# Optimization experiments

Measured on AMD Instinct MI355X. Metric: run time of the kernel, lower is better.

## Reference

```python
import jax, jax.numpy as jnp
import numpy as np

C_IN, C_OUT, K = 64, 64, 3
KK = K * K


def _conv3x3(x, w, b):
    # x: [B, Cin, H, W], w: [Cout, Cin, 3, 3], b: [Cout] or None. stride 1, pad 1.
    y = jax.lax.conv_general_dilated(
        x, w, window_strides=(1, 1), padding=((1, 1), (1, 1)),
        dimension_numbers=("NCHW", "OIHW", "NCHW"))
    if b is not None:
        y = y + b[None, :, None, None]
    return y


def _deform_conv2d(x, offset, mask, weight):
    # torchvision.ops.deform_conv2d with stride=1, pad=1, dilation=1, 1 offset group.
    # x: [B,C,H,W]; offset: [B,2*KK,H,W] (per-tap (dy,dx)); mask: [B,KK,H,W];
    # weight: [O,C,K,K]
    B, C, H, W = x.shape
    O = weight.shape[0]
    ky, kx = jnp.meshgrid(jnp.arange(K), jnp.arange(K), indexing="ij")
    hs = jnp.arange(H)
    ws = jnp.arange(W)
    # base sample positions per tap k=(ky*K+kx): [KK,H,W]
    base_y = (hs[:, None] - 1)[None] + ky.reshape(KK, 1, 1)
    base_x = (ws[None, :] - 1)[None] + kx.reshape(KK, 1, 1)
    off = offset.reshape(B, KK, 2, H, W)
    py = base_y[None].astype(x.dtype) + off[:, :, 0]  # [B,KK,H,W]
    px = base_x[None].astype(x.dtype) + off[:, :, 1]

    y0 = jnp.floor(py)
    x0 = jnp.floor(px)
    wy = py - y0  # bilinear fractional weights
    wx = px - x0
    y0i = y0.astype(jnp.int32)
    x0i = x0.astype(jnp.int32)

    imflat = x.reshape(B, C, H * W)

    def gather_b(im, idx):  # im: [C,HW], idx: [KK,H,W] -> [C,KK,H,W]
        return im[:, idx]

    val = jnp.zeros((B, C, KK, H, W), x.dtype)
    for dy, dx in ((0, 0), (0, 1), (1, 0), (1, 1)):
        yc = y0i + dy
        xc = x0i + dx
        valid = ((yc >= 0) & (yc < H) & (xc >= 0) & (xc < W)).astype(x.dtype)
        cw = (wy if dy else (1.0 - wy)) * (wx if dx else (1.0 - wx)) * valid
        idx = jnp.clip(yc, 0, H - 1) * W + jnp.clip(xc, 0, W - 1)
        g = jax.vmap(gather_b)(imflat, idx)  # [B,C,KK,H,W]
        val = val + cw[:, None] * g
    val = val * mask[:, None]  # modulation
    # contract 9-tap patches with conv weight
    return jnp.einsum("bckhw,ock->bohw", val, weight.reshape(O, C, KK))


def setup_inputs() -> dict:
    key = jax.random.key(0)
    ks = jax.random.split(key, 8)
    B, H, W = 4, 96, 96
    cin2 = 2 * C_IN + 2
    frame_i = jax.random.normal(ks[0], (B, C_IN, H, W), jnp.float32)
    frame_j = jax.random.normal(ks[1], (B, C_IN, H, W), jnp.float32)
    flow_ij = jax.random.normal(ks[2], (B, 2, H, W), jnp.float32)
    # small random weights so offsets are nonzero (zero-init would degenerate)
    w_off = jax.random.normal(ks[3], (2 * KK, cin2, K, K), jnp.float32) * 0.01
    b_off = jax.random.normal(ks[4], (2 * KK,), jnp.float32) * 0.1
    w_mod = jax.random.normal(ks[5], (KK, cin2, K, K), jnp.float32) * 0.01
    b_mod = jax.random.normal(ks[6], (KK,), jnp.float32) * 0.1
    w_reg = jax.random.normal(ks[7], (C_OUT, C_IN, K, K), jnp.float32) * (1.0 / np.sqrt(C_IN * KK))
    return {"frame_i": frame_i, "frame_j": frame_j, "flow_ij": flow_ij,
            "w_off": w_off, "b_off": b_off, "w_mod": w_mod, "b_mod": b_mod,
            "w_reg": w_reg}


def reference(frame_i, frame_j, flow_ij, w_off, b_off, w_mod, b_mod, w_reg):
    offset_input = jnp.concatenate([frame_i, frame_j, flow_ij], axis=1)
    offset = _conv3x3(offset_input, w_off, b_off)            # [B,2*KK,H,W]
    modulator = 2.0 * jax.nn.sigmoid(_conv3x3(offset_input, w_mod, b_mod))  # [B,KK,H,W]
    return _deform_conv2d(frame_j, offset, modulator, w_reg)
```

## Files before the change

kernel.cpp:

```cpp
#include <hip/hip_runtime.h>
#include <math.h>

#define BB   4
#define HH   96
#define WW   96
#define HW   (HH * WW)
#define CIN  64
#define COUT 64
#define C2B  192
#define NROW (BB * HW)
#define ZROW NROW
#define NSTRIP (NROW / 16)
#define BPX3 (NSTRIP / 8)
#define NA   (9 * 5 * 2 * 512)
#define NW   (9 * 2 * 4 * 512)
#define PXB2 (NROW / 32)
#define PWBLK 324
#define TSX  35
#define PR   55

typedef short v8s __attribute__((ext_vector_type(8)));
typedef float v4f __attribute__((ext_vector_type(4)));

__device__ __forceinline__ unsigned short f2bf(float f) {
    unsigned u = __float_as_uint(f);
    return (unsigned short)((u + 0x7FFFu + ((u >> 16) & 1u)) >> 16);
}
__device__ __forceinline__ unsigned pack2(float a, float b) {
    return (unsigned)f2bf(a) | ((unsigned)f2bf(b) << 16);
}
__device__ __forceinline__ unsigned bil2(unsigned a, unsigned b, unsigned c,
                                         unsigned d, float w00, float w01,
                                         float w10, float w11) {
    float lo = w00 * __uint_as_float(a << 16) + w01 * __uint_as_float(b << 16)
             + w10 * __uint_as_float(c << 16) + w11 * __uint_as_float(d << 16);
    float hi = w00 * __uint_as_float(a & 0xffff0000u)
             + w01 * __uint_as_float(b & 0xffff0000u)
             + w10 * __uint_as_float(c & 0xffff0000u)
             + w11 * __uint_as_float(d & 0xffff0000u);
    return pack2(lo, hi);
}

__global__ __launch_bounds__(256) void prep_kernel(
    const float* __restrict__ fi, const float* __restrict__ fj,
    const float* __restrict__ fl, const float* __restrict__ w_off,
    const float* __restrict__ w_mod, const float* __restrict__ w_reg,
    unsigned short* __restrict__ xt, unsigned short* __restrict__ wa2f,
    unsigned short* __restrict__ wb2f, uint4* __restrict__ vt)
{
    int blk = blockIdx.x;
    if (blk < PXB2) {
        __shared__ __align__(16) unsigned tile[64 * TSX];
        int tid = threadIdx.x;
        int p = tid & 63, cg = tid >> 6;
        int u = blk >> 1, half = blk & 1;
        int r0 = u * 64;
        int b = r0 / HW;
        int hwb = r0 - b * HW;
        int hw = hwb + p;
        uint4* dst = (uint4*)(xt + (size_t)r0 * C2B);
        if (half == 0) {
            const float* pi = fi + (size_t)b * CIN * HW + hw;
#pragma unroll
            for (int d = 0; d < 8; ++d) {
                int c = cg * 16 + 2 * d;
                tile[p * TSX + cg * 8 + d] =
                    pack2(pi[(size_t)c * HW], pi[(size_t)(c + 1) * HW]);
            }
            __syncthreads();
#pragma unroll
            for (int i = 0; i < 2; ++i) {
                int gq = i * 256 + tid;
                int rl = gq >> 3, c4 = gq & 7;
                const unsigned* s = &tile[rl * TSX + c4 * 4];
                uint4 v = {s[0], s[1], s[2], s[3]};
                dst[rl * 24 + c4] = v;
            }
        } else {
            const float* pj = fj + (size_t)b * CIN * HW + hw;
#pragma unroll
            for (int d = 0; d < 8; ++d) {
                int c = cg * 16 + 2 * d;
                tile[p * TSX + cg * 8 + d] =
                    pack2(pj[(size_t)c * HW], pj[(size_t)(c + 1) * HW]);
            }
            if (cg == 0) {
                const float* pf = fl + (size_t)b * 2 * HW + hw;
                tile[p * TSX + 32] = pack2(pf[0], pf[HW]);
            }
            __syncthreads();
#pragma unroll
            for (int i = 0; i < 4; ++i) {
                int gq = i * 256 + tid;
                int rl = gq >> 4, c4 = gq & 15;
                uint4 v = {0u, 0u, 0u, 0u};
                if (c4 < 8) {
                    const unsigned* s = &tile[rl * TSX + c4 * 4];
                    v.x = s[0]; v.y = s[1]; v.z = s[2]; v.w = s[3];
                } else if (c4 == 8) {
                    v.x = tile[rl * TSX + 32];
                }
                int pc4 = (c4 < 8) ? ((c4 & 3) * 2 + (c4 >> 2)) : c4;
                dst[rl * 24 + 8 + pc4] = v;
            }
#pragma unroll
            for (int i = 0; i < 2; ++i) {
                int it = i * 256 + tid;
                int pl = it >> 6, rl = it & 63;
                int o  = (pl >> 1) + (pl & 1) * 4;
                const unsigned* s = &tile[rl * TSX + o * 4];
                uint4 v = {s[0], s[1], s[2], s[3]};
                vt[((size_t)(b * 8 + pl)) * HW + hwb + rl] = v;
            }
        }
    } else if (blk < PXB2 + PWBLK) {
        int e = (blk - PXB2) * 256 + threadIdx.x;
        if (e < NA) {
            int t  = e / 5120;
            int r1 = e - t * 5120;
            int ks = r1 >> 10;
            int r2 = r1 & 1023;
            int nt = r2 >> 9;
            int l9 = r2 & 511;
            int l  = l9 >> 3, ee = l9 & 7;
            int m  = l & 15, g = l >> 4;
            int oc = nt * 16 + m;
            int ch = ks * 32 + g * 8 + ee;
            float v = 0.0f;
            if (oc < 27 && ch < 130) {
                if (oc < 18) v = w_off[((size_t)oc * 130 + ch) * 9 + t];
                else         v = w_mod[((size_t)(oc - 18) * 130 + ch) * 9 + t];
            }
            wa2f[e] = f2bf(v);
        } else {
            int e2 = e - NA;
            if (e2 < NW) {
                int k  = e2 >> 12;
                int r1 = e2 & 4095;
                int ks = r1 >> 11;
                int r2 = r1 & 2047;
                int nt = r2 >> 9;
                int l9 = r2 & 511;
                int l  = l9 >> 3, ee = l9 & 7;
                int m  = l & 15, g = l >> 4;
                int o  = nt * 16 + m;
                int c  = ks * 32 + g * 8 + ee;
                wb2f[e2] = f2bf(w_reg[((size_t)o * 64 + c) * 9 + k]);
            }
        }
    } else {
        if (threadIdx.x < 24) {
            uint4 z = {0u, 0u, 0u, 0u};
            ((uint4*)(xt + (size_t)ZROW * C2B))[threadIdx.x] = z;
        }
    }
}

__global__ __launch_bounds__(512, 8) void fused_kernel(
    const unsigned short* __restrict__ xt,
    const unsigned short* __restrict__ wa2f,
    const unsigned short* __restrict__ wb2f,
    const uint4* __restrict__ vt,
    const float* __restrict__ b_off, const float* __restrict__ b_mod,
    float* __restrict__ out)
{
    __shared__ __align__(16) unsigned char pool[17600];
    __shared__ __align__(16) float red1[8][8][64];
    __shared__ float lraw[16 * 28];

    uint4* patch4 = (uint4*)pool;
    float* red2   = (float*)pool;

    int l = threadIdx.x & 63;
    int wid = __builtin_amdgcn_readfirstlane(threadIdx.x >> 6);
    int m = l & 15, g = l >> 4;
    int strip = (blockIdx.x & 7) * BPX3 + (blockIdx.x >> 3);
    int b = strip / (HW / 16);
    int hw0 = (strip - b * (HW / 16)) * 16;
    int hw = hw0 + m;
    int x = hw % WW, y = hw / WW;
    int y0b = hw0 / WW, x0b = hw0 - y0b * WW;

#pragma unroll
    for (int i = 0; i < 3; ++i) {
        int item = i * 512 + threadIdx.x;
        if (item < 1080) {
            int run = item / 360;
            int rem = item - run * 360;
            int r18 = rem / 20;
            int c8  = rem - r18 * 20;
            int yy = y0b + run - 1;
            int xx = x0b - 1 + r18;
            bool ok = ((unsigned)yy < HH) && ((unsigned)xx < WW);
            uint4 v = {0u, 0u, 0u, 0u};
            if (ok)
                v = ((const uint4*)(xt + (size_t)(b * HW + yy * WW + xx) * C2B))[c8];
            patch4[c8 * PR + run * 18 + r18] = v;
        }
    }
    __syncthreads();

    v4f acc0 = {0.f, 0.f, 0.f, 0.f};
    v4f acc1 = {0.f, 0.f, 0.f, 0.f};
    {
        int nu = (wid < 5) ? 6 : 5;
#pragma unroll
        for (int i = 0; i < 6; ++i) {
            if (i < nu) {
                int u = wid + 8 * i;
                int t = u / 5, ks = u - 5 * t;
                int r = (t / 3) * 18 + (t % 3) + m;
                int c8 = (ks == 0) ? g : (ks == 1) ? 4 + g
                       : (ks == 2) ? 8 + 2 * g : (ks == 3) ? 9 + 2 * g
                       : 16 + g;
                v8s a = *(const v8s*)&patch4[c8 * PR + r];
                const unsigned short* wp =
                    wa2f + ((size_t)(u * 2)) * 512 + l * 8;
                v8s b0 = *(const v8s*)(wp);
                v8s b1 = *(const v8s*)(wp + 512);
                acc0 = __builtin_amdgcn_mfma_f32_16x16x32_bf16(a, b0, acc0, 0, 0, 0);
                acc1 = __builtin_amdgcn_mfma_f32_16x16x32_bf16(a, b1, acc1, 0, 0, 0);
            }
        }
    }

    {
#pragma unroll
        for (int j = 0; j < 4; ++j) red1[wid][j][l] = acc0[j];
#pragma unroll
        for (int j = 0; j < 4; ++j) red1[wid][4 + j][l] = acc1[j];
    }
    __syncthreads();

    {
        int j = wid;
        float v = 0.f;
#pragma unroll
        for (int sw = 0; sw < 8; ++sw) v += red1[sw][j][l];
        int r = j & 3;
        int oc = (j < 4) ? m : 16 + m;
        int pos = g * 4 + r;
        if (oc < 18) {
            lraw[pos * 28 + oc] = v + b_off[oc];
        } else if (oc < 27) {
            lraw[pos * 28 + oc] =
                2.0f / (1.0f + __expf(-(v + b_mod[oc - 18])));
        }
    }
    __syncthreads();

    v4f acc[4];
#pragma unroll
    for (int nt = 0; nt < 4; ++nt) acc[nt] = (v4f){0.f, 0.f, 0.f, 0.f};

    auto do_tap = [&](int k) {
        int ky = k / 3, kx = k - 3 * ky;
        float dy = lraw[m * 28 + 2 * k];
        float dx = lraw[m * 28 + 2 * k + 1];
        float mm = lraw[m * 28 + 18 + k];

        float py = (float)(y - 1 + ky) + dy;
        float px = (float)(x - 1 + kx) + dx;
        float fy = floorf(py), fx = floorf(px);
        int   y0 = (int)fy,    x0 = (int)fx;
        float wy = py - fy,    wx = px - fx;
        int   y1 = y0 + 1,     x1 = x0 + 1;

        bool y0v = (y0 >= 0) && (y0 < HH);
        bool y1v = (y1 >= 0) && (y1 < HH);
        bool x0v = (x0 >= 0) && (x0 < WW);
        bool x1v = (x1 >= 0) && (x1 < WW);

        float w00 = (1.f - wy) * (1.f - wx) * ((y0v && x0v) ? mm : 0.f);
        float w01 = (1.f - wy) * wx         * ((y0v && x1v) ? mm : 0.f);
        float w10 = wy * (1.f - wx)         * ((y1v && x0v) ? mm : 0.f);
        float w11 = wy * wx                 * ((y1v && x1v) ? mm : 0.f);

        int y0c = min(max(y0, 0), HH - 1), y1c = min(max(y1, 0), HH - 1);
        int x0c = min(max(x0, 0), WW - 1), x1c = min(max(x1, 0), WW - 1);
        int i00 = y0c * WW + x0c, i01 = y0c * WW + x1c;
        int i10 = y1c * WW + x0c, i11 = y1c * WW + x1c;

        const uint4* p0 = vt + ((size_t)(b * 8 + 2 * g + 0)) * HW;
        const uint4* p1 = vt + ((size_t)(b * 8 + 2 * g + 1)) * HW;

        uint4 a00 = p0[i00];
        uint4 a01 = p0[i01];
        uint4 a10 = p0[i10];
        uint4 a11 = p0[i11];
        uint4 c00 = p1[i00];
        uint4 c01 = p1[i01];
        uint4 c10 = p1[i10];
        uint4 c11 = p1[i11];

        uint4 ov0, ov1;
        ov0.x = bil2(a00.x, a01.x, a10.x, a11.x, w00, w01, w10, w11);
        ov0.y = bil2(a00.y, a01.y, a10.y, a11.y, w00, w01, w10, w11);
        ov0.z = bil2(a00.z, a01.z, a10.z, a11.z, w00, w01, w10, w11);
        ov0.w = bil2(a00.w, a01.w, a10.w, a11.w, w00, w01, w10, w11);
        ov1.x = bil2(c00.x, c01.x, c10.x, c11.x, w00, w01, w10, w11);
        ov1.y = bil2(c00.y, c01.y, c10.y, c11.y, w00, w01, w10, w11);
        ov1.z = bil2(c00.z, c01.z, c10.z, c11.z, w00, w01, w10, w11);
        ov1.w = bil2(c00.w, c01.w, c10.w, c11.w, w00, w01, w10, w11);
        v8s af0 = __builtin_bit_cast(v8s, ov0);
        v8s af1 = __builtin_bit_cast(v8s, ov1);

#pragma unroll
        for (int nt = 0; nt < 4; ++nt) {
            const unsigned short* wp0 =
                wb2f + ((size_t)((k * 2 + 0) * 4 + nt)) * 512 + l * 8;
            const unsigned short* wp1 =
                wb2f + ((size_t)((k * 2 + 1) * 4 + nt)) * 512 + l * 8;
            v8s bb0 = *(const v8s*)wp0;
            v8s bb1 = *(const v8s*)wp1;
            acc[nt] = __builtin_amdgcn_mfma_f32_16x16x32_bf16(af0, bb0, acc[nt], 0, 0, 0);
            acc[nt] = __builtin_amdgcn_mfma_f32_16x16x32_bf16(af1, bb1, acc[nt], 0, 0, 0);
        }
    };

    auto do_half = [&](int k, int ks) {
        int ky = k / 3, kx = k - 3 * ky;
        float dy = lraw[m * 28 + 2 * k];
        float dx = lraw[m * 28 + 2 * k + 1];
        float mm = lraw[m * 28 + 18 + k];

        float py = (float)(y - 1 + ky) + dy;
        float px = (float)(x - 1 + kx) + dx;
        float fy = floorf(py), fx = floorf(px);
        int   y0 = (int)fy,    x0 = (int)fx;
        float wy = py - fy,    wx = px - fx;
        int   y1 = y0 + 1,     x1 = x0 + 1;

        bool y0v = (y0 >= 0) && (y0 < HH);
        bool y1v = (y1 >= 0) && (y1 < HH);
        bool x0v = (x0 >= 0) && (x0 < WW);
        bool x1v = (x1 >= 0) && (x1 < WW);

        float w00 = (1.f - wy) * (1.f - wx) * ((y0v && x0v) ? mm : 0.f);
        float w01 = (1.f - wy) * wx         * ((y0v && x1v) ? mm : 0.f);
        float w10 = wy * (1.f - wx)         * ((y1v && x0v) ? mm : 0.f);
        float w11 = wy * wx                 * ((y1v && x1v) ? mm : 0.f);

        int y0c = min(max(y0, 0), HH - 1), y1c = min(max(y1, 0), HH - 1);
        int x0c = min(max(x0, 0), WW - 1), x1c = min(max(x1, 0), WW - 1);
        int i00 = y0c * WW + x0c, i01 = y0c * WW + x1c;
        int i10 = y1c * WW + x0c, i11 = y1c * WW + x1c;

        const uint4* pk = vt + ((size_t)(b * 8 + 2 * g + ks)) * HW;
        uint4 a00 = pk[i00];
        uint4 a01 = pk[i01];
        uint4 a10 = pk[i10];
        uint4 a11 = pk[i11];

        uint4 ov;
        ov.x = bil2(a00.x, a01.x, a10.x, a11.x, w00, w01, w10, w11);
        ov.y = bil2(a00.y, a01.y, a10.y, a11.y, w00, w01, w10, w11);
        ov.z = bil2(a00.z, a01.z, a10.z, a11.z, w00, w01, w10, w11);
        ov.w = bil2(a00.w, a01.w, a10.w, a11.w, w00, w01, w10, w11);
        v8s af = __builtin_bit_cast(v8s, ov);

#pragma unroll
        for (int nt = 0; nt < 4; ++nt) {
            const unsigned short* wp =
                wb2f + ((size_t)((k * 2 + ks) * 4 + nt)) * 512 + l * 8;
            v8s bb = *(const v8s*)wp;
            acc[nt] = __builtin_amdgcn_mfma_f32_16x16x32_bf16(af, bb, acc[nt], 0, 0, 0);
        }
    };

    do_tap(wid);
    if (wid == 6) do_half(8, 0);
    if (wid == 7) do_half(8, 1);

    if (wid >= 4) {
        float* rb = red2 + ((size_t)(wid - 4) * 16) * 64;
#pragma unroll
        for (int nt = 0; nt < 4; ++nt)
#pragma unroll
            for (int r = 0; r < 4; ++r)
                rb[(nt * 4 + r) * 64 + l] = acc[nt][r];
    }
    __syncthreads();
    if (wid < 4) {
        float* rb = red2 + ((size_t)wid * 16) * 64;
#pragma unroll
        for (int nt = 0; nt < 4; ++nt)
#pragma unroll
            for (int r = 0; r < 4; ++r) {
                float t = rb[(nt * 4 + r) * 64 + l] + acc[nt][r];
                rb[(nt * 4 + r) * 64 + l] = t;
            }
    }
    __syncthreads();
    {
        int nt = wid >> 1, r0 = (wid & 1) * 2;
        float v0 = 0.f, v1 = 0.f;
#pragma unroll
        for (int bu = 0; bu < 4; ++bu) {
            v0 += red2[((size_t)bu * 16 + nt * 4 + r0) * 64 + l];
            v1 += red2[((size_t)bu * 16 + nt * 4 + r0 + 1) * 64 + l];
        }
        float* op = out + ((size_t)(b * COUT + nt * 16 + m)) * HW
                  + hw0 + g * 4 + r0;
        float2 s2 = {v0, v1};
        *(float2*)op = s2;
    }
}

extern "C" void kernel_launch(void* const* d_in, const int* in_sizes, int n_in,
                              void* d_out, int out_size, void* d_ws, size_t ws_size,
                              hipStream_t stream)
{
    const float* frame_i = (const float*)d_in[0];
    const float* frame_j = (const float*)d_in[1];
    const float* flow_ij = (const float*)d_in[2];
    const float* w_off   = (const float*)d_in[3];
    const float* b_off   = (const float*)d_in[4];
    const float* w_mod   = (const float*)d_in[5];
    const float* b_mod   = (const float*)d_in[6];
    const float* w_reg   = (const float*)d_in[7];
    float* out = (float*)d_out;

    unsigned short* xt   = (unsigned short*)d_ws;
    unsigned short* wa2f = xt + (size_t)(NROW + 1) * C2B;
    unsigned short* wb2f = wa2f + NA;
    uint4* vt            = (uint4*)(wb2f + NW);

    prep_kernel<<<PXB2 + PWBLK + 1, 256, 0, stream>>>(
        frame_i, frame_j, flow_ij, w_off, w_mod, w_reg, xt, wa2f, wb2f, vt);

    fused_kernel<<<NSTRIP, 512, 0, stream>>>(
        xt, wa2f, wb2f, vt, b_off, b_mod, out);
}
```

Baseline: 115.3 us.

## Make fused kernel persistent over three strips with register-prefetched patches

The fused kernel now launches 768 blocks, each handling three 16-pixel strips in a loop instead of one strip per block. The input patch for the next strip is loaded into registers while the current strip computes, so global load latency overlaps with MFMA and gather work. The cost is extra registers for the prefetch (launch bounds lowered from 8 to 6), an extra barrier per iteration, and less parallelism across blocks.

Result: slower. 202.9 us (+76.0%).

```diff
diff --git a/kernel.cpp b/kernel.cpp
--- a/kernel.cpp
+++ b/kernel.cpp
@@ -12,6 +12,7 @@
 #define ZROW NROW
 #define NSTRIP (NROW / 16)
 #define BPX3 (NSTRIP / 8)
+#define GRID 768
 #define NA   (9 * 5 * 2 * 512)
 #define NW   (9 * 2 * 4 * 512)
 #define PXB2 (NROW / 32)
@@ -156,7 +157,7 @@
     }
 }
 
-__global__ __launch_bounds__(512, 8) void fused_kernel(
+__global__ __launch_bounds__(512, 6) void fused_kernel(
     const unsigned short* __restrict__ xt,
     const unsigned short* __restrict__ wa2f,
     const unsigned short* __restrict__ wb2f,
@@ -171,239 +172,275 @@
     uint4* patch4 = (uint4*)pool;
     float* red2   = (float*)pool;
 
-    int l = threadIdx.x & 63;
-    int wid = __builtin_amdgcn_readfirstlane(threadIdx.x >> 6);
+    int tid = threadIdx.x;
+    int l = tid & 63;
+    int wid = __builtin_amdgcn_readfirstlane(tid >> 6);
     int m = l & 15, g = l >> 4;
-    int strip = (blockIdx.x & 7) * BPX3 + (blockIdx.x >> 3);
-    int b = strip / (HW / 16);
-    int hw0 = (strip - b * (HW / 16)) * 16;
-    int hw = hw0 + m;
-    int x = hw % WW, y = hw / WW;
-    int y0b = hw0 / WW, x0b = hw0 - y0b * WW;
-
-#pragma unroll
+    int bx = blockIdx.x;
+
+    int it0 = tid, it1 = tid + 512, it2 = tid + 1024;
+    int run0 = it0 / 360, rm0 = it0 - run0 * 360;
+    int r180 = rm0 / 20,  c80 = rm0 - r180 * 20;
+    int run1 = it1 / 360, rm1 = it1 - run1 * 360;
+    int r181 = rm1 / 20,  c81 = rm1 - r181 * 20;
+    int run2 = it2 / 360, rm2 = it2 - run2 * 360;
+    int r182 = rm2 / 20,  c82 = rm2 - r182 * 20;
+    int lo0 = c80 * PR + run0 * 18 + r180;
+    int lo1 = c81 * PR + run1 * 18 + r181;
+    int lo2 = c82 * PR + run2 * 18 + r182;
+
+    auto ld_item = [&](int b, int y0b, int x0b, int run, int r18, int c8) {
+        int yy = y0b + run - 1;
+        int xx = x0b - 1 + r18;
+        bool ok = ((unsigned)yy < HH) && ((unsigned)xx < WW);
+        uint4 v = {0u, 0u, 0u, 0u};
+        if (ok)
+            v = ((const uint4*)(xt + (size_t)(b * HW + yy * WW + xx) * C2B))[c8];
+        return v;
+    };
+
+    auto geom = [&](int sj, int& b, int& hw0) {
+        int strip = (sj & 7) * BPX3 + (sj >> 3);
+        b = strip / (HW / 16);
+        hw0 = (strip - b * (HW / 16)) * 16;
+    };
+
+    uint4 pf0, pf1, pf2;
+    {
+        int b, hw0; geom(bx, b, hw0);
+        int y0b = hw0 / WW, x0b = hw0 - y0b * WW;
+        pf0 = ld_item(b, y0b, x0b, run0, r180, c80);
+        pf1 = ld_item(b, y0b, x0b, run1, r181, c81);
+        pf2 = (tid < 56) ? ld_item(b, y0b, x0b, run2, r182, c82)
+                         : (uint4){0u, 0u, 0u, 0u};
+    }
+
+#pragma unroll 1
     for (int i = 0; i < 3; ++i) {
-        int item = i * 512 + threadIdx.x;
-        if (item < 1080) {
-            int run = item / 360;
-            int rem = item - run * 360;
-            int r18 = rem / 20;
-            int c8  = rem - r18 * 20;
-            int yy = y0b + run - 1;
-            int xx = x0b - 1 + r18;
-            bool ok = ((unsigned)yy < HH) && ((unsigned)xx < WW);
-            uint4 v = {0u, 0u, 0u, 0u};
-            if (ok)
-                v = ((const uint4*)(xt + (size_t)(b * HW + yy * WW + xx) * C2B))[c8];
-            patch4[c8 * PR + run * 18 + r18] = v;
-        }
-    }
-    __syncthreads();
-
-    v4f acc0 = {0.f, 0.f, 0.f, 0.f};
-    v4f acc1 = {0.f, 0.f, 0.f, 0.f};
-    {
-        int nu = (wid < 5) ? 6 : 5;
-#pragma unroll
-        for (int i = 0; i < 6; ++i) {
-            if (i < nu) {
-                int u = wid + 8 * i;
-                int t = u / 5, ks = u - 5 * t;
-                int r = (t / 3) * 18 + (t % 3) + m;
-                int c8 = (ks == 0) ? g : (ks == 1) ? 4 + g
-                       : (ks == 2) ? 8 + 2 * g : (ks == 3) ? 9 + 2 * g
-                       : 16 + g;
-                v8s a = *(const v8s*)&patch4[c8 * PR + r];
+        int sj = bx + i * GRID;
+        int b, hw0; geom(sj, b, hw0);
+        int hw = hw0 + m;
+        int x = hw % WW, y = hw / WW;
+
+        patch4[lo0] = pf0;
+        patch4[lo1] = pf1;
+        if (tid < 56) patch4[lo2] = pf2;
+        __syncthreads();
+
+        if (i < 2) {
+            int bn, hn; geom(sj + GRID, bn, hn);
+            int y0n = hn / WW, x0n = hn - y0n * WW;
+            pf0 = ld_item(bn, y0n, x0n, run0, r180, c80);
+            pf1 = ld_item(bn, y0n, x0n, run1, r181, c81);
+            if (tid < 56) pf2 = ld_item(bn, y0n, x0n, run2, r182, c82);
+        }
+
+        v4f acc0 = {0.f, 0.f, 0.f, 0.f};
+        v4f acc1 = {0.f, 0.f, 0.f, 0.f};
+        {
+            int nu = (wid < 5) ? 6 : 5;
+#pragma unroll
+            for (int ii = 0; ii < 6; ++ii) {
+                if (ii < nu) {
+                    int u = wid + 8 * ii;
+                    int t = u / 5, ks = u - 5 * t;
+                    int r = (t / 3) * 18 + (t % 3) + m;
+                    int c8 = (ks == 0) ? g : (ks == 1) ? 4 + g
+                           : (ks == 2) ? 8 + 2 * g : (ks == 3) ? 9 + 2 * g
+                           : 16 + g;
+                    v8s a = *(const v8s*)&patch4[c8 * PR + r];
+                    const unsigned short* wp =
+                        wa2f + ((size_t)(u * 2)) * 512 + l * 8;
+                    v8s b0 = *(const v8s*)(wp);
+                    v8s b1 = *(const v8s*)(wp + 512);
+                    acc0 = __builtin_amdgcn_mfma_f32_16x16x32_bf16(a, b0, acc0, 0, 0, 0);
+                    acc1 = __builtin_amdgcn_mfma_f32_16x16x32_bf16(a, b1, acc1, 0, 0, 0);
+                }
+            }
+        }
+
+        {
+#pragma unroll
+            for (int j = 0; j < 4; ++j) red1[wid][j][l] = acc0[j];
+#pragma unroll
+            for (int j = 0; j < 4; ++j) red1[wid][4 + j][l] = acc1[j];
+        }
+        __syncthreads();
+
+        {
+            int j = wid;
+            float v = 0.f;
+#pragma unroll
+            for (int sw = 0; sw < 8; ++sw) v += red1[sw][j][l];
+            int r = j & 3;
+            int oc = (j < 4) ? m : 16 + m;
+            int pos = g * 4 + r;
+            if (oc < 18) {
+                lraw[pos * 28 + oc] = v + b_off[oc];
+            } else if (oc < 27) {
+                lraw[pos * 28 + oc] =
+                    2.0f / (1.0f + __expf(-(v + b_mod[oc - 18])));
+            }
+        }
+        __syncthreads();
+
+        v4f acc[4];
+#pragma unroll
+        for (int nt = 0; nt < 4; ++nt) acc[nt] = (v4f){0.f, 0.f, 0.f, 0.f};
+
+        auto do_tap = [&](int k) {
+            int ky = k / 3, kx = k - 3 * ky;
+            float dy = lraw[m * 28 + 2 * k];
+            float dx = lraw[m * 28 + 2 * k + 1];
+            float mm = lraw[m * 28 + 18 + k];
+
+            float py = (float)(y - 1 + ky) + dy;
+            float px = (float)(x - 1 + kx) + dx;
+            float fy = floorf(py), fx = floorf(px);
+            int   y0 = (int)fy,    x0 = (int)fx;
+            float wy = py - fy,    wx = px - fx;
+            int   y1 = y0 + 1,     x1 = x0 + 1;
+
+            bool y0v = (y0 >= 0) && (y0 < HH);
+            bool y1v = (y1 >= 0) && (y1 < HH);
+            bool x0v = (x0 >= 0) && (x0 < WW);
+            bool x1v = (x1 >= 0) && (x1 < WW);
+
+            float w00 = (1.f - wy) * (1.f - wx) * ((y0v && x0v) ? mm : 0.f);
+            float w01 = (1.f - wy) * wx         * ((y0v && x1v) ? mm : 0.f);
+            float w10 = wy * (1.f - wx)         * ((y1v && x0v) ? mm : 0.f);
+            float w11 = wy * wx                 * ((y1v && x1v) ? mm : 0.f);
+
+            int y0c = min(max(y0, 0), HH - 1), y1c = min(max(y1, 0), HH - 1);
+            int x0c = min(max(x0, 0), WW - 1), x1c = min(max(x1, 0), WW - 1);
+            int i00 = y0c * WW + x0c, i01 = y0c * WW + x1c;
+            int i10 = y1c * WW + x0c, i11 = y1c * WW + x1c;
+
+            const uint4* p0 = vt + ((size_t)(b * 8 + 2 * g + 0)) * HW;
+            const uint4* p1 = vt + ((size_t)(b * 8 + 2 * g + 1)) * HW;
+
+            uint4 a00 = p0[i00];
+            uint4 a01 = p0[i01];
+            uint4 a10 = p0[i10];
+            uint4 a11 = p0[i11];
+            uint4 c00 = p1[i00];
+            uint4 c01 = p1[i01];
+            uint4 c10 = p1[i10];
+            uint4 c11 = p1[i11];
+
+            uint4 ov0, ov1;
+            ov0.x = bil2(a00.x, a01.x, a10.x, a11.x, w00, w01, w10, w11);
+            ov0.y = bil2(a00.y, a01.y, a10.y, a11.y, w00, w01, w10, w11);
+            ov0.z = bil2(a00.z, a01.z, a10.z, a11.z, w00, w01, w10, w11);
+            ov0.w = bil2(a00.w, a01.w, a10.w, a11.w, w00, w01, w10, w11);
+            ov1.x = bil2(c00.x, c01.x, c10.x, c11.x, w00, w01, w10, w11);
+            ov1.y = bil2(c00.y, c01.y, c10.y, c11.y, w00, w01, w10, w11);
+            ov1.z = bil2(c00.z, c01.z, c10.z, c11.z, w00, w01, w10, w11);
+            ov1.w = bil2(c00.w, c01.w, c10.w, c11.w, w00, w01, w10, w11);
+            v8s af0 = __builtin_bit_cast(v8s, ov0);
+            v8s af1 = __builtin_bit_cast(v8s, ov1);
+
+#pragma unroll
+            for (int nt = 0; nt < 4; ++nt) {
+                const unsigned short* wp0 =
+                    wb2f + ((size_t)((k * 2 + 0) * 4 + nt)) * 512 + l * 8;
+                const unsigned short* wp1 =
+                    wb2f + ((size_t)((k * 2 + 1) * 4 + nt)) * 512 + l * 8;
+                v8s bb0 = *(const v8s*)wp0;
+                v8s bb1 = *(const v8s*)wp1;
+                acc[nt] = __builtin_amdgcn_mfma_f32_16x16x32_bf16(af0, bb0, acc[nt], 0, 0, 0);
+                acc[nt] = __builtin_amdgcn_mfma_f32_16x16x32_bf16(af1, bb1, acc[nt], 0, 0, 0);
+            }
+        };
+
+        auto do_half = [&](int k, int ks) {
+            int ky = k / 3, kx = k - 3 * ky;
+            float dy = lraw[m * 28 + 2 * k];
+            float dx = lraw[m * 28 + 2 * k + 1];
+            float mm = lraw[m * 28 + 18 + k];
+
+            float py = (float)(y - 1 + ky) + dy;
+            float px = (float)(x - 1 + kx) + dx;
+            float fy = floorf(py), fx = floorf(px);
+            int   y0 = (int)fy,    x0 = (int)fx;
+            float wy = py - fy,    wx = px - fx;
+            int   y1 = y0 + 1,     x1 = x0 + 1;
+
+            bool y0v = (y0 >= 0) && (y0 < HH);
+            bool y1v = (y1 >= 0) && (y1 < HH);
+            bool x0v = (x0 >= 0) && (x0 < WW);
+            bool x1v = (x1 >= 0) && (x1 < WW);
+
+            float w00 = (1.f - wy) * (1.f - wx) * ((y0v && x0v) ? mm : 0.f);
+            float w01 = (1.f - wy) * wx         * ((y0v && x1v) ? mm : 0.f);
+            float w10 = wy * (1.f - wx)         * ((y1v && x0v) ? mm : 0.f);
+            float w11 = wy * wx                 * ((y1v && x1v) ? mm : 0.f);
+
+            int y0c = min(max(y0, 0), HH - 1), y1c = min(max(y1, 0), HH - 1);
+            int x0c = min(max(x0, 0), WW - 1), x1c = min(max(x1, 0), WW - 1);
+            int i00 = y0c * WW + x0c, i01 = y0c * WW + x1c;
+            int i10 = y1c * WW + x0c, i11 = y1c * WW + x1c;
+
+            const uint4* pk = vt + ((size_t)(b * 8 + 2 * g + ks)) * HW;
+            uint4 a00 = pk[i00];
+            uint4 a01 = pk[i01];
+            uint4 a10 = pk[i10];
+            uint4 a11 = pk[i11];
+
+            uint4 ov;
+            ov.x = bil2(a00.x, a01.x, a10.x, a11.x, w00, w01, w10, w11);
+            ov.y = bil2(a00.y, a01.y, a10.y, a11.y, w00, w01, w10, w11);
+            ov.z = bil2(a00.z, a01.z, a10.z, a11.z, w00, w01, w10, w11);
+            ov.w = bil2(a00.w, a01.w, a10.w, a11.w, w00, w01, w10, w11);
+            v8s af = __builtin_bit_cast(v8s, ov);
+
+#pragma unroll
+            for (int nt = 0; nt < 4; ++nt) {
                 const unsigned short* wp =
-                    wa2f + ((size_t)(u * 2)) * 512 + l * 8;
-                v8s b0 = *(const v8s*)(wp);
-                v8s b1 = *(const v8s*)(wp + 512);
-                acc0 = __builtin_amdgcn_mfma_f32_16x16x32_bf16(a, b0, acc0, 0, 0, 0);
-                acc1 = __builtin_amdgcn_mfma_f32_16x16x32_bf16(a, b1, acc1, 0, 0, 0);
-            }
-        }
-    }
-
-    {
-#pragma unroll
-        for (int j = 0; j < 4; ++j) red1[wid][j][l] = acc0[j];
-#pragma unroll
-        for (int j = 0; j < 4; ++j) red1[wid][4 + j][l] = acc1[j];
-    }
-    __syncthreads();
-
-    {
-        int j = wid;
-        float v = 0.f;
-#pragma unroll
-        for (int sw = 0; sw < 8; ++sw) v += red1[sw][j][l];
-        int r = j & 3;
-        int oc = (j < 4) ? m : 16 + m;
-        int pos = g * 4 + r;
-        if (oc < 18) {
-            lraw[pos * 28 + oc] = v + b_off[oc];
-        } else if (oc < 27) {
-            lraw[pos * 28 + oc] =
-                2.0f / (1.0f + __expf(-(v + b_mod[oc - 18])));
-        }
-    }
-    __syncthreads();
-
-    v4f acc[4];
-#pragma unroll
-    for (int nt = 0; nt < 4; ++nt) acc[nt] = (v4f){0.f, 0.f, 0.f, 0.f};
-
-    auto do_tap = [&](int k) {
-        int ky = k / 3, kx = k - 3 * ky;
-        float dy = lraw[m * 28 + 2 * k];
-        float dx = lraw[m * 28 + 2 * k + 1];
-        float mm = lraw[m * 28 + 18 + k];
-
-        float py = (float)(y - 1 + ky) + dy;
-        float px = (float)(x - 1 + kx) + dx;
-        float fy = floorf(py), fx = floorf(px);
-        int   y0 = (int)fy,    x0 = (int)fx;
-        float wy = py - fy,    wx = px - fx;
-        int   y1 = y0 + 1,     x1 = x0 + 1;
-
-        bool y0v = (y0 >= 0) && (y0 < HH);
-        bool y1v = (y1 >= 0) && (y1 < HH);
-        bool x0v = (x0 >= 0) && (x0 < WW);
-        bool x1v = (x1 >= 0) && (x1 < WW);
-
-        float w00 = (1.f - wy) * (1.f - wx) * ((y0v && x0v) ? mm : 0.f);
-        float w01 = (1.f - wy) * wx         * ((y0v && x1v) ? mm : 0.f);
-        float w10 = wy * (1.f - wx)         * ((y1v && x0v) ? mm : 0.f);
-        float w11 = wy * wx                 * ((y1v && x1v) ? mm : 0.f);
-
-        int y0c = min(max(y0, 0), HH - 1), y1c = min(max(y1, 0), HH - 1);
-        int x0c = min(max(x0, 0), WW - 1), x1c = min(max(x1, 0), WW - 1);
-        int i00 = y0c * WW + x0c, i01 = y0c * WW + x1c;
-        int i10 = y1c * WW + x0c, i11 = y1c * WW + x1c;
-
-        const uint4* p0 = vt + ((size_t)(b * 8 + 2 * g + 0)) * HW;
-        const uint4* p1 = vt + ((size_t)(b * 8 + 2 * g + 1)) * HW;
-
-        uint4 a00 = p0[i00];
-        uint4 a01 = p0[i01];
-        uint4 a10 = p0[i10];
-        uint4 a11 = p0[i11];
-        uint4 c00 = p1[i00];
-        uint4 c01 = p1[i01];
-        uint4 c10 = p1[i10];
-        uint4 c11 = p1[i11];
-
-        uint4 ov0, ov1;
-        ov0.x = bil2(a00.x, a01.x, a10.x, a11.x, w00, w01, w10, w11);
-        ov0.y = bil2(a00.y, a01.y, a10.y, a11.y, w00, w01, w10, w11);
-        ov0.z = bil2(a00.z, a01.z, a10.z, a11.z, w00, w01, w10, w11);
-        ov0.w = bil2(a00.w, a01.w, a10.w, a11.w, w00, w01, w10, w11);
-        ov1.x = bil2(c00.x, c01.x, c10.x, c11.x, w00, w01, w10, w11);
-        ov1.y = bil2(c00.y, c01.y, c10.y, c11.y, w00, w01, w10, w11);
-        ov1.z = bil2(c00.z, c01.z, c10.z, c11.z, w00, w01, w10, w11);
-        ov1.w = bil2(c00.w, c01.w, c10.w, c11.w, w00, w01, w10, w11);
-        v8s af0 = __builtin_bit_cast(v8s, ov0);
-        v8s af1 = __builtin_bit_cast(v8s, ov1);
-
-#pragma unroll
-        for (int nt = 0; nt < 4; ++nt) {
-            const unsigned short* wp0 =
-                wb2f + ((size_t)((k * 2 + 0) * 4 + nt)) * 512 + l * 8;
-            const unsigned short* wp1 =
-                wb2f + ((size_t)((k * 2 + 1) * 4 + nt)) * 512 + l * 8;
-            v8s bb0 = *(const v8s*)wp0;
-            v8s bb1 = *(const v8s*)wp1;
-            acc[nt] = __builtin_amdgcn_mfma_f32_16x16x32_bf16(af0, bb0, acc[nt], 0, 0, 0);
-            acc[nt] = __builtin_amdgcn_mfma_f32_16x16x32_bf16(af1, bb1, acc[nt], 0, 0, 0);
-        }
-    };
-
-    auto do_half = [&](int k, int ks) {
-        int ky = k / 3, kx = k - 3 * ky;
-        float dy = lraw[m * 28 + 2 * k];
-        float dx = lraw[m * 28 + 2 * k + 1];
-        float mm = lraw[m * 28 + 18 + k];
-
-        float py = (float)(y - 1 + ky) + dy;
-        float px = (float)(x - 1 + kx) + dx;
-        float fy = floorf(py), fx = floorf(px);
-        int   y0 = (int)fy,    x0 = (int)fx;
-        float wy = py - fy,    wx = px - fx;
-        int   y1 = y0 + 1,     x1 = x0 + 1;
-
-        bool y0v = (y0 >= 0) && (y0 < HH);
-        bool y1v = (y1 >= 0) && (y1 < HH);
-        bool x0v = (x0 >= 0) && (x0 < WW);
-        bool x1v = (x1 >= 0) && (x1 < WW);
-
-        float w00 = (1.f - wy) * (1.f - wx) * ((y0v && x0v) ? mm : 0.f);
-        float w01 = (1.f - wy) * wx         * ((y0v && x1v) ? mm : 0.f);
-        float w10 = wy * (1.f - wx)         * ((y1v && x0v) ? mm : 0.f);
-        float w11 = wy * wx                 * ((y1v && x1v) ? mm : 0.f);
-
-        int y0c = min(max(y0, 0), HH - 1), y1c = min(max(y1, 0), HH - 1);
-        int x0c = min(max(x0, 0), WW - 1), x1c = min(max(x1, 0), WW - 1);
-        int i00 = y0c * WW + x0c, i01 = y0c * WW + x1c;
-        int i10 = y1c * WW + x0c, i11 = y1c * WW + x1c;
-
-        const uint4* pk = vt + ((size_t)(b * 8 + 2 * g + ks)) * HW;
-        uint4 a00 = pk[i00];
-        uint4 a01 = pk[i01];
-        uint4 a10 = pk[i10];
-        uint4 a11 = pk[i11];
-
-        uint4 ov;
-        ov.x = bil2(a00.x, a01.x, a10.x, a11.x, w00, w01, w10, w11);
-        ov.y = bil2(a00.y, a01.y, a10.y, a11.y, w00, w01, w10, w11);
-        ov.z = bil2(a00.z, a01.z, a10.z, a11.z, w00, w01, w10, w11);
-        ov.w = bil2(a00.w, a01.w, a10.w, a11.w, w00, w01, w10, w11);
-        v8s af = __builtin_bit_cast(v8s, ov);
-
-#pragma unroll
-        for (int nt = 0; nt < 4; ++nt) {
-            const unsigned short* wp =
-                wb2f + ((size_t)((k * 2 + ks) * 4 + nt)) * 512 + l * 8;
-            v8s bb = *(const v8s*)wp;
-            acc[nt] = __builtin_amdgcn_mfma_f32_16x16x32_bf16(af, bb, acc[nt], 0, 0, 0);
-        }
-    };
-
-    do_tap(wid);
-    if (wid == 6) do_half(8, 0);
-    if (wid == 7) do_half(8, 1);
-
-    if (wid >= 4) {
-        float* rb = red2 + ((size_t)(wid - 4) * 16) * 64;
-#pragma unroll
-        for (int nt = 0; nt < 4; ++nt)
-#pragma unroll
-            for (int r = 0; r < 4; ++r)
-                rb[(nt * 4 + r) * 64 + l] = acc[nt][r];
-    }
-    __syncthreads();
-    if (wid < 4) {
-        float* rb = red2 + ((size_t)wid * 16) * 64;
-#pragma unroll
-        for (int nt = 0; nt < 4; ++nt)
-#pragma unroll
-            for (int r = 0; r < 4; ++r) {
-                float t = rb[(nt * 4 + r) * 64 + l] + acc[nt][r];
-                rb[(nt * 4 + r) * 64 + l] = t;
-            }
-    }
-    __syncthreads();
-    {
-        int nt = wid >> 1, r0 = (wid & 1) * 2;
-        float v0 = 0.f, v1 = 0.f;
-#pragma unroll
-        for (int bu = 0; bu < 4; ++bu) {
-            v0 += red2[((size_t)bu * 16 + nt * 4 + r0) * 64 + l];
-            v1 += red2[((size_t)bu * 16 + nt * 4 + r0 + 1) * 64 + l];
-        }
-        float* op = out + ((size_t)(b * COUT + nt * 16 + m)) * HW
-                  + hw0 + g * 4 + r0;
-        float2 s2 = {v0, v1};
-        *(float2*)op = s2;
+                    wb2f + ((size_t)((k * 2 + ks) * 4 + nt)) * 512 + l * 8;
+                v8s bb = *(const v8s*)wp;
+                acc[nt] = __builtin_amdgcn_mfma_f32_16x16x32_bf16(af, bb, acc[nt], 0, 0, 0);
+            }
+        };
+
+        do_tap(wid);
+        if (wid == 6) do_half(8, 0);
+        if (wid == 7) do_half(8, 1);
+
+        if (wid >= 4) {
+            float* rb = red2 + ((size_t)(wid - 4) * 16) * 64;
+#pragma unroll
+            for (int nt = 0; nt < 4; ++nt)
+#pragma unroll
+                for (int r = 0; r < 4; ++r)
+                    rb[(nt * 4 + r) * 64 + l] = acc[nt][r];
+        }
+        __syncthreads();
+        if (wid < 4) {
+            float* rb = red2 + ((size_t)wid * 16) * 64;
+#pragma unroll
+            for (int nt = 0; nt < 4; ++nt)
+#pragma unroll
+                for (int r = 0; r < 4; ++r) {
+                    float t = rb[(nt * 4 + r) * 64 + l] + acc[nt][r];
+                    rb[(nt * 4 + r) * 64 + l] = t;
+                }
+        }
+        __syncthreads();
+        {
+            int nt = wid >> 1, r0 = (wid & 1) * 2;
+            float v0 = 0.f, v1 = 0.f;
+#pragma unroll
+            for (int bu = 0; bu < 4; ++bu) {
+                v0 += red2[((size_t)bu * 16 + nt * 4 + r0) * 64 + l];
+                v1 += red2[((size_t)bu * 16 + nt * 4 + r0 + 1) * 64 + l];
+            }
+            float* op = out + ((size_t)(b * COUT + nt * 16 + m)) * HW
+                      + hw0 + g * 4 + r0;
+            float2 s2 = {v0, v1};
+            *(float2*)op = s2;
+        }
+        __syncthreads();
     }
 }
 
@@ -429,6 +466,6 @@
     prep_kernel<<<PXB2 + PWBLK + 1, 256, 0, stream>>>(
         frame_i, frame_j, flow_ij, w_off, w_mod, w_reg, xt, wa2f, wb2f, vt);
 
-    fused_kernel<<<NSTRIP, 512, 0, stream>>>(
+    fused_kernel<<<GRID, 512, 0, stream>>>(
         xt, wa2f, wb2f, vt, b_off, b_mod, out);
 }
```

## Unify activation staging into planar bf16 layout shared by conv and deform sampling

Applied to the files above, without the earlier changes.

Replaces the row-major 192-wide bf16 activation buffer plus the separate planar frame_j copy with a single per-batch planar layout of 17 planes (each one uint4 of 8 channels per pixel), with a zero pixel appended per plane. The prep kernel now writes frame_j planes once instead of twice, and the fused kernel loads its conv patch and its bilinear gathers from the same buffer. This cuts prep write traffic and workspace size, and shrinks the shared patch. In exchange, patch loads become per-plane gathers with different coalescing, and the flow plane now pads a full uint4 per pixel.

Result: faster. 112.1 us (-2.8%).

```diff
diff --git a/kernel.cpp b/kernel.cpp
--- a/kernel.cpp
+++ b/kernel.cpp
@@ -7,9 +7,9 @@
 #define HW   (HH * WW)
 #define CIN  64
 #define COUT 64
-#define C2B  192
+#define NPL  17
+#define HWP  (HW + 1)
 #define NROW (BB * HW)
-#define ZROW NROW
 #define NSTRIP (NROW / 16)
 #define BPX3 (NSTRIP / 8)
 #define NA   (9 * 5 * 2 * 512)
@@ -17,7 +17,7 @@
 #define PXB2 (NROW / 32)
 #define PWBLK 324
 #define TSX  35
-#define PR   55
+#define NIT  (NPL * 54)
 
 typedef short v8s __attribute__((ext_vector_type(8)));
 typedef float v4f __attribute__((ext_vector_type(4)));
@@ -45,8 +45,8 @@
     const float* __restrict__ fi, const float* __restrict__ fj,
     const float* __restrict__ fl, const float* __restrict__ w_off,
     const float* __restrict__ w_mod, const float* __restrict__ w_reg,
-    unsigned short* __restrict__ xt, unsigned short* __restrict__ wa2f,
-    unsigned short* __restrict__ wb2f, uint4* __restrict__ vt)
+    uint4* __restrict__ xp, unsigned short* __restrict__ wa2f,
+    unsigned short* __restrict__ wb2f)
 {
     int blk = blockIdx.x;
     if (blk < PXB2) {
@@ -58,7 +58,7 @@
         int b = r0 / HW;
         int hwb = r0 - b * HW;
         int hw = hwb + p;
-        uint4* dst = (uint4*)(xt + (size_t)r0 * C2B);
+        uint4* xpb = xp + (size_t)b * NPL * HWP;
         if (half == 0) {
             const float* pi = fi + (size_t)b * CIN * HW + hw;
 #pragma unroll
@@ -70,11 +70,11 @@
             __syncthreads();
 #pragma unroll
             for (int i = 0; i < 2; ++i) {
-                int gq = i * 256 + tid;
-                int rl = gq >> 3, c4 = gq & 7;
-                const unsigned* s = &tile[rl * TSX + c4 * 4];
+                int it = i * 256 + tid;
+                int pl = it >> 6, rl = it & 63;
+                const unsigned* s = &tile[rl * TSX + pl * 4];
                 uint4 v = {s[0], s[1], s[2], s[3]};
-                dst[rl * 24 + c4] = v;
+                xpb[(size_t)pl * HWP + hwb + rl] = v;
             }
         } else {
             const float* pj = fj + (size_t)b * CIN * HW + hw;
@@ -89,20 +89,6 @@
                 tile[p * TSX + 32] = pack2(pf[0], pf[HW]);
             }
             __syncthreads();
-#pragma unroll
-            for (int i = 0; i < 4; ++i) {
-                int gq = i * 256 + tid;
-                int rl = gq >> 4, c4 = gq & 15;
-                uint4 v = {0u, 0u, 0u, 0u};
-                if (c4 < 8) {
-                    const unsigned* s = &tile[rl * TSX + c4 * 4];
-                    v.x = s[0]; v.y = s[1]; v.z = s[2]; v.w = s[3];
-                } else if (c4 == 8) {
-                    v.x = tile[rl * TSX + 32];
-                }
-                int pc4 = (c4 < 8) ? ((c4 & 3) * 2 + (c4 >> 2)) : c4;
-                dst[rl * 24 + 8 + pc4] = v;
-            }
 #pragma unroll
             for (int i = 0; i < 2; ++i) {
                 int it = i * 256 + tid;
@@ -110,7 +96,11 @@
                 int o  = (pl >> 1) + (pl & 1) * 4;
                 const unsigned* s = &tile[rl * TSX + o * 4];
                 uint4 v = {s[0], s[1], s[2], s[3]};
-                vt[((size_t)(b * 8 + pl)) * HW + hwb + rl] = v;
+                xpb[(size_t)(8 + pl) * HWP + hwb + rl] = v;
+            }
+            if (tid < 64) {
+                uint4 v = {tile[tid * TSX + 32], 0u, 0u, 0u};
+                xpb[(size_t)16 * HWP + hwb + tid] = v;
             }
         }
     } else if (blk < PXB2 + PWBLK) {
@@ -149,30 +139,31 @@
             }
         }
     } else {
-        if (threadIdx.x < 24) {
+        if (threadIdx.x < BB * NPL) {
+            int bz = threadIdx.x / NPL, pl = threadIdx.x - bz * NPL;
             uint4 z = {0u, 0u, 0u, 0u};
-            ((uint4*)(xt + (size_t)ZROW * C2B))[threadIdx.x] = z;
+            xp[((size_t)bz * NPL + pl) * HWP + HW] = z;
         }
     }
 }
 
 __global__ __launch_bounds__(512, 8) void fused_kernel(
-    const unsigned short* __restrict__ xt,
+    const uint4* __restrict__ xp,
     const unsigned short* __restrict__ wa2f,
     const unsigned short* __restrict__ wb2f,
-    const uint4* __restrict__ vt,
     const float* __restrict__ b_off, const float* __restrict__ b_mod,
     float* __restrict__ out)
 {
-    __shared__ __align__(16) unsigned char pool[17600];
+    __shared__ __align__(16) unsigned char pool[16384];
     __shared__ __align__(16) float red1[8][8][64];
     __shared__ float lraw[16 * 28];
 
-    uint4* patch4 = (uint4*)pool;
+    uint4* patchL = (uint4*)pool;
     float* red2   = (float*)pool;
 
-    int l = threadIdx.x & 63;
-    int wid = __builtin_amdgcn_readfirstlane(threadIdx.x >> 6);
+    int tid = threadIdx.x;
+    int l = tid & 63;
+    int wid = __builtin_amdgcn_readfirstlane(tid >> 6);
     int m = l & 15, g = l >> 4;
     int strip = (blockIdx.x & 7) * BPX3 + (blockIdx.x >> 3);
     int b = strip / (HW / 16);
@@ -181,21 +172,21 @@
     int x = hw % WW, y = hw / WW;
     int y0b = hw0 / WW, x0b = hw0 - y0b * WW;
 
-#pragma unroll
-    for (int i = 0; i < 3; ++i) {
-        int item = i * 512 + threadIdx.x;
-        if (item < 1080) {
-            int run = item / 360;
-            int rem = item - run * 360;
-            int r18 = rem / 20;
-            int c8  = rem - r18 * 20;
+    const uint4* xpb = xp + (size_t)b * NPL * HWP;
+
+#pragma unroll
+    for (int i = 0; i < 2; ++i) {
+        int item = i * 512 + tid;
+        if (item < NIT) {
+            int pl  = item / 54;
+            int rm  = item - pl * 54;
+            int run = rm / 18;
+            int r18 = rm - run * 18;
             int yy = y0b + run - 1;
             int xx = x0b - 1 + r18;
             bool ok = ((unsigned)yy < HH) && ((unsigned)xx < WW);
-            uint4 v = {0u, 0u, 0u, 0u};
-            if (ok)
-                v = ((const uint4*)(xt + (size_t)(b * HW + yy * WW + xx) * C2B))[c8];
-            patch4[c8 * PR + run * 18 + r18] = v;
+            int pos = ok ? (yy * WW + xx) : HW;
+            patchL[item] = xpb[(size_t)pl * HWP + pos];
         }
     }
     __syncthreads();
@@ -210,10 +201,16 @@
                 int u = wid + 8 * i;
                 int t = u / 5, ks = u - 5 * t;
                 int r = (t / 3) * 18 + (t % 3) + m;
-                int c8 = (ks == 0) ? g : (ks == 1) ? 4 + g
-                       : (ks == 2) ? 8 + 2 * g : (ks == 3) ? 9 + 2 * g
-                       : 16 + g;
-                v8s a = *(const v8s*)&patch4[c8 * PR + r];
+                v8s a;
+                if (ks == 4) {
+                    uint4 t4 = patchL[16 * 54 + r];
+                    if (g) t4 = (uint4){0u, 0u, 0u, 0u};
+                    a = __builtin_bit_cast(v8s, t4);
+                } else {
+                    int pl = (ks == 0) ? g : (ks == 1) ? 4 + g
+                           : (ks == 2) ? 8 + 2 * g : 9 + 2 * g;
+                    a = *(const v8s*)&patchL[pl * 54 + r];
+                }
                 const unsigned short* wp =
                     wa2f + ((size_t)(u * 2)) * 512 + l * 8;
                 v8s b0 = *(const v8s*)(wp);
@@ -281,8 +278,8 @@
         int i00 = y0c * WW + x0c, i01 = y0c * WW + x1c;
         int i10 = y1c * WW + x0c, i11 = y1c * WW + x1c;
 
-        const uint4* p0 = vt + ((size_t)(b * 8 + 2 * g + 0)) * HW;
-        const uint4* p1 = vt + ((size_t)(b * 8 + 2 * g + 1)) * HW;
+        const uint4* p0 = xpb + (size_t)(8 + 2 * g) * HWP;
+        const uint4* p1 = p0 + HWP;
 
         uint4 a00 = p0[i00];
         uint4 a01 = p0[i01];
@@ -346,7 +343,7 @@
         int i00 = y0c * WW + x0c, i01 = y0c * WW + x1c;
         int i10 = y1c * WW + x0c, i11 = y1c * WW + x1c;
 
-        const uint4* pk = vt + ((size_t)(b * 8 + 2 * g + ks)) * HW;
+        const uint4* pk = xpb + (size_t)(8 + 2 * g + ks) * HWP;
         uint4 a00 = pk[i00];
         uint4 a01 = pk[i01];
         uint4 a10 = pk[i10];
@@ -421,14 +418,13 @@
     const float* w_reg   = (const float*)d_in[7];
     float* out = (float*)d_out;
 
-    unsigned short* xt   = (unsigned short*)d_ws;
-    unsigned short* wa2f = xt + (size_t)(NROW + 1) * C2B;
+    uint4* xp = (uint4*)d_ws;
+    unsigned short* wa2f = (unsigned short*)(xp + (size_t)BB * NPL * HWP);
     unsigned short* wb2f = wa2f + NA;
-    uint4* vt            = (uint4*)(wb2f + NW);
 
     prep_kernel<<<PXB2 + PWBLK + 1, 256, 0, stream>>>(
-        frame_i, frame_j, flow_ij, w_off, w_mod, w_reg, xt, wa2f, wb2f, vt);
+        frame_i, frame_j, flow_ij, w_off, w_mod, w_reg, xp, wa2f, wb2f);
 
     fused_kernel<<<NSTRIP, 512, 0, stream>>>(
-        xt, wa2f, wb2f, vt, b_off, b_mod, out);
-}
+        xp, wa2f, wb2f, b_off, b_mod, out);
+}
```
